# Performance work log

Hardware: AMD Instinct MI355X
Metric: run time of the kernel (lower is better)

## Reference

```python
import jax, jax.numpy as jnp
import numpy as np

N = 100_000   # nodes
E = 1_600_000 # edges (avg degree 16)
IN = 256
OUT = 128
NEG_SLOPE = 0.01  # torch F.leaky_relu default


def setup_inputs() -> dict:
    key = jax.random.key(0)
    k1, k2, k3, k4, k5 = jax.random.split(key, 5)
    h = jax.random.normal(k1, (N, IN), dtype=jnp.float32)
    W = jax.random.normal(k2, (IN, OUT), dtype=jnp.float32) * 0.05  # fc weight (in->out)
    a = jax.random.normal(k3, (2 * OUT,), dtype=jnp.float32) * 0.05  # attn_fc weight, flattened
    src = jax.random.randint(k4, (E,), 0, N, dtype=jnp.int32)
    dst = jax.random.randint(k5, (E,), 0, N, dtype=jnp.int32)
    return {"h": h, "W": W, "a": a, "src": src, "dst": dst, "counter": 3}


def reference(h, W, a, src, dst, counter):
    out_dim = W.shape[1]
    z = h @ W                               # [N, OUT] = fc(h)
    # edge_attention: e = leaky_relu(attn_fc(cat(z[src], z[dst])))
    s = z @ a[:out_dim]                     # [N] src contribution
    t = z @ a[out_dim:]                     # [N] dst contribution
    e = jax.nn.leaky_relu(s[src] + t[dst], NEG_SLOPE)  # [E]
    # segment softmax over incoming edges of each dst node (fixed across iterations)
    m = jax.ops.segment_max(e, dst, num_segments=N)    # [N]
    w = jnp.exp(e - m[dst])                             # [E]
    denom = jax.ops.segment_sum(w, dst, num_segments=N)  # [N]
    alpha = w / denom[dst]                               # [E]
    # nodes with no in-edges keep their previous h (DGL update_all semantics)
    deg = jax.ops.segment_sum(jnp.ones_like(e), dst, num_segments=N)
    has_in = (deg > 0)[:, None]                          # [N,1]
    hcur = z
    for _ in range(int(counter)):
        agg = jax.ops.segment_sum(alpha[:, None] * hcur[src], dst, num_segments=N)  # [N,OUT]
        hcur = jnp.where(has_in, agg, hcur)
    return hcur
```

## Files before the change

### kernel.cpp

```cpp
#include <hip/hip_runtime.h>
#include <math.h>

#define IN_DIM 256
#define OUT_DIM 128
#define BK 1024
#define NBMAX 128

typedef _Float16 f16;
typedef _Float16 f16x2 __attribute__((ext_vector_type(2)));
typedef _Float16 f16x8 __attribute__((ext_vector_type(8)));
typedef float    f32x4 __attribute__((ext_vector_type(4)));

static inline size_t align256(size_t x){ return (x + 255) & ~size_t(255); }

__global__ void init_kernel(int* __restrict__ gcount, int NB){
  int i = threadIdx.x;
  if (i < NB) gcount[i] = 0;
}

__global__ __launch_bounds__(256) void wprep_kernel(const float* __restrict__ Wm,
    f16* __restrict__ WThi, f16* __restrict__ WTlo){
  int idx = blockIdx.x*256 + threadIdx.x;
  int k = idx >> 7, n = idx & 127;
  float v = Wm[(size_t)k*OUT_DIM + n];
  f16 hi = (f16)v;
  WThi[(size_t)n*IN_DIM + k] = hi;
  WTlo[(size_t)n*IN_DIM + k] = (f16)(v - (float)hi);
}

__global__ __launch_bounds__(256) void gemm_kernel(const float* __restrict__ h,
    const f16* __restrict__ WThi, const f16* __restrict__ WTlo,
    const float* __restrict__ attn_a,
    float* __restrict__ z, f16* __restrict__ zh,
    float* __restrict__ s_arr, float* __restrict__ t_arr, int N){
  __shared__ float spart[128][2];
  __shared__ float tpart[128][2];

  const int t = threadIdx.x;
  const int l = t & 63;
  const int w = t >> 6;
  const int wr = w >> 1;
  const int wc = w & 1;
  const int m15 = l & 15;
  const int g   = l >> 4;
  const int row0 = blockIdx.x * 128;

  const float* hrow[4];
  #pragma unroll
  for (int rt=0; rt<4; rt++){
    int r = row0 + wr*64 + rt*16 + m15;
    if (r > N-1) r = N-1;
    hrow[rt] = h + (size_t)r*IN_DIM;
  }
  const f16* bhp[4]; const f16* blp[4];
  #pragma unroll
  for (int ct=0; ct<4; ct++){
    int n = wc*64 + ct*16 + m15;
    bhp[ct] = WThi + (size_t)n*IN_DIM;
    blp[ct] = WTlo + (size_t)n*IN_DIM;
  }

  f32x4 acc[4][4];
  #pragma unroll
  for (int i=0;i<4;i++)
    #pragma unroll
    for (int j=0;j<4;j++) acc[i][j] = (f32x4){0.f,0.f,0.f,0.f};

  const int g8 = g*8;
  #pragma unroll 2
  for (int k0 = 0; k0 < IN_DIM; k0 += 32){
    f16x8 ah[4], al[4];
    #pragma unroll
    for (int rt=0;rt<4;rt++){
      float4 v0 = *(const float4*)&hrow[rt][k0+g8];
      float4 v1 = *(const float4*)&hrow[rt][k0+g8+4];
      float vv[8] = {v0.x,v0.y,v0.z,v0.w,v1.x,v1.y,v1.z,v1.w};
      f16x8 hh, ll;
      #pragma unroll
      for (int q=0;q<8;q++){
        f16 hq = (f16)vv[q];
        hh[q] = hq;
        ll[q] = (f16)(vv[q] - (float)hq);
      }
      ah[rt] = hh; al[rt] = ll;
    }
    #pragma unroll
    for (int ct=0;ct<4;ct++){
      f16x8 bh = *(const f16x8*)&bhp[ct][k0+g8];
      f16x8 bl = *(const f16x8*)&blp[ct][k0+g8];
      #pragma unroll
      for (int rt=0;rt<4;rt++){
        acc[rt][ct] = __builtin_amdgcn_mfma_f32_16x16x32_f16(ah[rt], bh, acc[rt][ct], 0, 0, 0);
        acc[rt][ct] = __builtin_amdgcn_mfma_f32_16x16x32_f16(ah[rt], bl, acc[rt][ct], 0, 0, 0);
        acc[rt][ct] = __builtin_amdgcn_mfma_f32_16x16x32_f16(al[rt], bh, acc[rt][ct], 0, 0, 0);
      }
    }
  }

  float as_[4], at_[4];
  #pragma unroll
  for (int ct=0; ct<4; ct++){
    as_[ct] = attn_a[wc*64 + ct*16 + m15];
    at_[ct] = attn_a[OUT_DIM + wc*64 + ct*16 + m15];
  }

  #pragma unroll
  for (int rt=0; rt<4; rt++){
    #pragma unroll
    for (int r=0; r<4; r++){
      int lrow = wr*64 + rt*16 + g*4 + r;
      int grow = row0 + lrow;
      float sp = 0.f, tp = 0.f;
      #pragma unroll
      for (int ct=0; ct<4; ct++){
        float v = acc[rt][ct][r];
        if (grow < N){
          z [(size_t)grow*OUT_DIM + wc*64 + ct*16 + m15] = v;
          zh[(size_t)grow*OUT_DIM + wc*64 + ct*16 + m15] = (f16)v;
        }
        sp = fmaf(v, as_[ct], sp);
        tp = fmaf(v, at_[ct], tp);
      }
      #pragma unroll
      for (int o=1; o<16; o<<=1){ sp += __shfl_xor(sp,o); tp += __shfl_xor(tp,o); }
      if (m15 == 0){ spart[lrow][wc] = sp; tpart[lrow][wc] = tp; }
    }
  }
  __syncthreads();
  if (t < 128){
    int grow = row0 + t;
    if (grow < N){
      s_arr[grow] = spart[t][0] + spart[t][1];
      t_arr[grow] = tpart[t][0] + tpart[t][1];
    }
  }
}

__global__ __launch_bounds__(256) void count_kernel(const int* __restrict__ dst,
    int* __restrict__ gcount, int E, int NB){
  __shared__ int lh[NBMAX];
  for (int i=threadIdx.x; i<NB; i+=256) lh[i]=0;
  __syncthreads();
  int i = blockIdx.x*blockDim.x + threadIdx.x;
  int stride = gridDim.x*blockDim.x;
  for (; i<E; i+=stride) atomicAdd(&lh[dst[i]>>10], 1);
  __syncthreads();
  for (int i=threadIdx.x; i<NB; i+=256){
    int c = lh[i];
    if (c) atomicAdd(&gcount[i], c);
  }
}

__global__ __launch_bounds__(128) void scanb_kernel(const int* __restrict__ gcount,
    int* __restrict__ gbase, int* __restrict__ gcursor, int* __restrict__ offs,
    int NB, int N, int E){
  int tid = threadIdx.x;
  int v = (tid < NB) ? gcount[tid] : 0;
  int lane = tid & 63, wv = tid >> 6;
  int x = v;
  #pragma unroll
  for (int o=1;o<64;o<<=1){ int y = __shfl_up(x,o); if (lane>=o) x += y; }
  __shared__ int wt[2];
  if (lane==63) wt[wv] = x;
  __syncthreads();
  int off = wv ? wt[0] : 0;
  int excl = off + x - v;
  if (tid < NB){ gbase[tid] = excl; gcursor[tid] = excl; }
  if (tid == 0){ gbase[NB] = E; offs[N] = E; }
}

__global__ __launch_bounds__(256) void scatter_kernel(const int* __restrict__ src,
    const int* __restrict__ dst, const float* __restrict__ s_arr,
    const float* __restrict__ t_arr, int* __restrict__ gcursor,
    int* __restrict__ p_sd, float* __restrict__ p_w, int E, int NB){
  __shared__ int lh[NBMAX];
  __shared__ int lbase[NBMAX];
  for (int i=threadIdx.x;i<NB;i+=256) lh[i]=0;
  __syncthreads();
  int base = blockIdx.x * (256*8);
  int sN[8], dN[8], rk[8];
  float wv[8];
  #pragma unroll
  for (int k=0;k<8;k++){
    int j = base + threadIdx.x + k*256;
    if (j < E){
      int s_ = src[j], d_ = dst[j];
      float e = s_arr[s_] + t_arr[d_];
      e = e > 0.f ? e : 0.01f*e;
      wv[k] = __expf(e);
      sN[k] = s_; dN[k] = d_;
      rk[k] = atomicAdd(&lh[d_>>10], 1);
    } else rk[k] = -1;
  }
  __syncthreads();
  for (int i=threadIdx.x;i<NB;i+=256){
    int c = lh[i];
    lbase[i] = c ? atomicAdd(&gcursor[i], c) : 0;
  }
  __syncthreads();
  #pragma unroll
  for (int k=0;k<8;k++){
    if (rk[k] >= 0){
      int b = dN[k] >> 10;
      int pos = lbase[b] + rk[k];
      p_sd[pos] = sN[k] | ((dN[k] & 1023) << 20);
      p_w[pos]  = wv[k];
    }
  }
}

__global__ __launch_bounds__(512) void bucket_kernel(const int* __restrict__ gbase,
    const int* __restrict__ p_sd, const float* __restrict__ p_w,
    int* __restrict__ offs, int2* __restrict__ csrp, int N){
  __shared__ int   hist[BK];
  __shared__ float wsum[BK];
  __shared__ int   loff[BK];
  __shared__ int   wtot[8];
  int b = blockIdx.x;
  int tid = threadIdx.x;
  int e0 = gbase[b], e1 = gbase[b+1];
  int n0 = b << 10;
  int nn = min(BK, N - n0);
  for (int i=tid;i<BK;i+=512){ hist[i]=0; wsum[i]=0.f; }
  __syncthreads();
  for (int j=e0+tid; j<e1; j+=512){
    int dl = p_sd[j] >> 20;
    atomicAdd(&hist[dl], 1);
    atomicAdd(&wsum[dl], p_w[j]);
  }
  __syncthreads();
  int v0 = hist[tid*2], v1 = hist[tid*2+1];
  int tsum = v0 + v1;
  int lane = tid & 63, wv = tid >> 6;
  int x = tsum;
  #pragma unroll
  for (int o=1;o<64;o<<=1){ int y = __shfl_up(x,o); if (lane>=o) x += y; }
  if (lane==63) wtot[wv] = x;
  __syncthreads();
  int woff = 0;
  for (int i=0;i<wv;i++) woff += wtot[i];
  int excl = woff + x - tsum;
  if (tid*2   < nn) offs[n0 + tid*2  ] = e0 + excl;
  loff[tid*2] = excl; excl += v0;
  if (tid*2+1 < nn) offs[n0 + tid*2+1] = e0 + excl;
  loff[tid*2+1] = excl;
  __syncthreads();
  for (int j=e0+tid; j<e1; j+=512){
    int sd = p_sd[j];
    int dl = sd >> 20;
    int r = atomicAdd(&loff[dl], 1);
    int2 pk; pk.x = sd & 0xFFFFF; pk.y = __float_as_int(p_w[j] / wsum[dl]);
    csrp[e0 + r] = pk;
  }
}

__global__ __launch_bounds__(256) void agg_kernel(const f16* __restrict__ hIn,
    f16* __restrict__ hOut, const float* __restrict__ z, float* __restrict__ out,
    const int* __restrict__ offs, const int2* __restrict__ csrp,
    const int* __restrict__ counter, int it, int N){
  int wv   = threadIdx.x >> 6;
  int lane = threadIdx.x & 63;
  int n = blockIdx.x*4 + wv;
  if (n >= N) return;
  int cntr = counter[0];
  if (cntr <= 0){
    if (it == 0)
      *(float2*)&out[(size_t)n*OUT_DIM + lane*2] =
        *(const float2*)&z[(size_t)n*OUT_DIM + lane*2];
    return;
  }
  if (it >= cntr) return;
  const bool fin = (it == cntr - 1);
  int s0 = offs[n], s1 = offs[n+1];
  if (s0 == s1){
    if (fin)
      *(float2*)&out[(size_t)n*OUT_DIM + lane*2] =
        *(const float2*)&z[(size_t)n*OUT_DIM + lane*2];
    else
      *(f16x2*)&hOut[(size_t)n*OUT_DIM + lane*2] =
        *(const f16x2*)&hIn[(size_t)n*OUT_DIM + lane*2];
    return;
  }
  float2 a0c = {0.f,0.f}, a1c = {0.f,0.f}, a2c = {0.f,0.f}, a3c = {0.f,0.f};
  for (int base = s0; base < s1; base += 64){
    int j = base + lane;
    int2 me = make_int2(0, 0);
    if (j < s1) me = csrp[j];
    int cnt = min(64, s1 - base);
    int k = 0;
    for (; k+4 <= cnt; k += 4){
      int sk0 = __shfl(me.x, k+0); float w0 = __int_as_float(__shfl(me.y, k+0));
      int sk1 = __shfl(me.x, k+1); float w1 = __int_as_float(__shfl(me.y, k+1));
      int sk2 = __shfl(me.x, k+2); float w2 = __int_as_float(__shfl(me.y, k+2));
      int sk3 = __shfl(me.x, k+3); float w3 = __int_as_float(__shfl(me.y, k+3));
      f16x2 v0 = *(const f16x2*)&hIn[(size_t)sk0*OUT_DIM + lane*2];
      f16x2 v1 = *(const f16x2*)&hIn[(size_t)sk1*OUT_DIM + lane*2];
      f16x2 v2 = *(const f16x2*)&hIn[(size_t)sk2*OUT_DIM + lane*2];
      f16x2 v3 = *(const f16x2*)&hIn[(size_t)sk3*OUT_DIM + lane*2];
      a0c.x = fmaf(w0, (float)v0.x, a0c.x); a0c.y = fmaf(w0, (float)v0.y, a0c.y);
      a1c.x = fmaf(w1, (float)v1.x, a1c.x); a1c.y = fmaf(w1, (float)v1.y, a1c.y);
      a2c.x = fmaf(w2, (float)v2.x, a2c.x); a2c.y = fmaf(w2, (float)v2.y, a2c.y);
      a3c.x = fmaf(w3, (float)v3.x, a3c.x); a3c.y = fmaf(w3, (float)v3.y, a3c.y);
    }
    for (; k < cnt; k++){
      int sk = __shfl(me.x, k); float wk = __int_as_float(__shfl(me.y, k));
      f16x2 v = *(const f16x2*)&hIn[(size_t)sk*OUT_DIM + lane*2];
      a0c.x = fmaf(wk, (float)v.x, a0c.x); a0c.y = fmaf(wk, (float)v.y, a0c.y);
    }
  }
  float2 res;
  res.x = (a0c.x + a1c.x) + (a2c.x + a3c.x);
  res.y = (a0c.y + a1c.y) + (a2c.y + a3c.y);
  if (fin){
    *(float2*)&out[(size_t)n*OUT_DIM + lane*2] = res;
  } else {
    f16x2 o = {(f16)res.x, (f16)res.y};
    *(f16x2*)&hOut[(size_t)n*OUT_DIM + lane*2] = o;
  }
}

extern "C" void kernel_launch(void* const* d_in, const int* in_sizes, int n_in,
                              void* d_out, int out_size, void* d_ws, size_t ws_size,
                              hipStream_t stream){
  const float* h   = (const float*)d_in[0];
  const float* Wm  = (const float*)d_in[1];
  const float* a   = (const float*)d_in[2];
  const int*   src = (const int*)d_in[3];
  const int*   dst = (const int*)d_in[4];
  const int* counter = (const int*)d_in[5];
  const int N = in_sizes[0] / IN_DIM;
  const int E = in_sizes[3];
  const int NB = (N + BK - 1) / BK;
  float* out = (float*)d_out;

  char* p = (char*)d_ws;
  auto alloc = [&](size_t bytes){ void* r = (void*)p; p += align256(bytes); return r; };
  float* z         = (float*)alloc((size_t)N*OUT_DIM*4);
  f16*   hA        = (f16*)  alloc((size_t)N*OUT_DIM*2);
  f16*   hB        = (f16*)  alloc((size_t)N*OUT_DIM*2);
  float* s_arr     = (float*)alloc((size_t)N*4);
  float* t_arr     = (float*)alloc((size_t)N*4);
  int*   p_sd      = (int*)  alloc((size_t)E*4);
  float* p_w       = (float*)alloc((size_t)E*4);
  int2*  csrp      = (int2*) alloc((size_t)E*8);
  int*   offs      = (int*)  alloc((size_t)(N+1)*4);
  int*   gcount    = (int*)  alloc((size_t)NBMAX*4);
  int*   gbase     = (int*)  alloc((size_t)(NBMAX+1)*4);
  int*   gcursor   = (int*)  alloc((size_t)NBMAX*4);
  f16*   WThi      = (f16*)  alloc((size_t)IN_DIM*OUT_DIM*2);
  f16*   WTlo      = (f16*)  alloc((size_t)IN_DIM*OUT_DIM*2);

  init_kernel<<<1, 128, 0, stream>>>(gcount, NB);
  wprep_kernel<<<(IN_DIM*OUT_DIM)/256, 256, 0, stream>>>(Wm, WThi, WTlo);
  gemm_kernel<<<(N+127)/128, 256, 0, stream>>>(h, WThi, WTlo, a, z, hA, s_arr, t_arr, N);
  count_kernel<<<512, 256, 0, stream>>>(dst, gcount, E, NB);
  scanb_kernel<<<1, 128, 0, stream>>>(gcount, gbase, gcursor, offs, NB, N, E);
  scatter_kernel<<<(E + 2047)/2048, 256, 0, stream>>>(src, dst, s_arr, t_arr,
                                                      gcursor, p_sd, p_w, E, NB);
  bucket_kernel<<<NB, 512, 0, stream>>>(gbase, p_sd, p_w, offs, csrp, N);
  agg_kernel<<<(N+3)/4, 256, 0, stream>>>(hA, hB, z, out, offs, csrp, counter, 0, N);
  agg_kernel<<<(N+3)/4, 256, 0, stream>>>(hB, hA, z, out, offs, csrp, counter, 1, N);
  agg_kernel<<<(N+3)/4, 256, 0, stream>>>(hA, hB, z, out, offs, csrp, counter, 2, N);
}
```

Measured before the change: 383.0 us.

## Stage GEMM A-tiles in LDS, drop fp32 z buffer, halve bucket size

The GEMM now loads each h row once per block, converts it to hi/lo fp16 and double-buffers it in shared memory. Before, each wave reread and reconverted h rows straight from global memory. The fp32 z output is removed, so nodes without in-edges (and the counter<=0 case) now output the fp16 copy upcast to float. This cuts about 51MB of writes but loses precision on those rows. Bucket size drops from 1024 to 512 nodes, doubling the number of bucket blocks, and the scan and bucket kernels are adjusted to match.

Result: faster. 335.7 us (-12.3%).

```diff
diff --git a/kernel.cpp b/kernel.cpp
--- a/kernel.cpp
+++ b/kernel.cpp
@@ -3,8 +3,8 @@
 
 #define IN_DIM 256
 #define OUT_DIM 128
-#define BK 1024
-#define NBMAX 128
+#define BK 512
+#define NBMAX 256
 
 typedef _Float16 f16;
 typedef _Float16 f16x2 __attribute__((ext_vector_type(2)));
@@ -31,8 +31,8 @@
 __global__ __launch_bounds__(256) void gemm_kernel(const float* __restrict__ h,
     const f16* __restrict__ WThi, const f16* __restrict__ WTlo,
     const float* __restrict__ attn_a,
-    float* __restrict__ z, f16* __restrict__ zh,
-    float* __restrict__ s_arr, float* __restrict__ t_arr, int N){
+    f16* __restrict__ zh, float* __restrict__ s_arr, float* __restrict__ t_arr, int N){
+  __shared__ f16x8 Alds[2][2][512];
   __shared__ float spart[128][2];
   __shared__ float tpart[128][2];
 
@@ -45,13 +45,11 @@
   const int g   = l >> 4;
   const int row0 = blockIdx.x * 128;
 
-  const float* hrow[4];
-  #pragma unroll
-  for (int rt=0; rt<4; rt++){
-    int r = row0 + wr*64 + rt*16 + m15;
-    if (r > N-1) r = N-1;
-    hrow[rt] = h + (size_t)r*IN_DIM;
-  }
+  const int srow = t >> 1;
+  const int g0 = (t & 1) * 2;
+  const float* srcrow = h + (size_t)min(row0 + srow, N-1) * IN_DIM;
+  const int wslot0 = (srow >> 4)*64 + g0*16 + (srow & 15);
+
   const f16* bhp[4]; const f16* blp[4];
   #pragma unroll
   for (int ct=0; ct<4; ct++){
@@ -66,35 +64,64 @@
     #pragma unroll
     for (int j=0;j<4;j++) acc[i][j] = (f32x4){0.f,0.f,0.f,0.f};
 
-  const int g8 = g*8;
-  #pragma unroll 2
-  for (int k0 = 0; k0 < IN_DIM; k0 += 32){
+  auto cvt_write = [&](int buf, float4* r){
+    float vv[16] = {r[0].x,r[0].y,r[0].z,r[0].w, r[1].x,r[1].y,r[1].z,r[1].w,
+                    r[2].x,r[2].y,r[2].z,r[2].w, r[3].x,r[3].y,r[3].z,r[3].w};
+    f16x8 hh0, ll0, hh1, ll1;
+    #pragma unroll
+    for (int q=0;q<8;q++){
+      f16 a = (f16)vv[q];   hh0[q]=a; ll0[q]=(f16)(vv[q]  -(float)a);
+      f16 c = (f16)vv[q+8]; hh1[q]=c; ll1[q]=(f16)(vv[q+8]-(float)c);
+    }
+    Alds[buf][0][wslot0]    = hh0;
+    Alds[buf][1][wslot0]    = ll0;
+    Alds[buf][0][wslot0+16] = hh1;
+    Alds[buf][1][wslot0+16] = ll1;
+  };
+
+  float4 rg4[2][4];
+  #pragma unroll
+  for (int q=0;q<4;q++) rg4[0][q] = *(const float4*)&srcrow[g0*8 + q*4];
+  cvt_write(0, rg4[0]);
+  #pragma unroll
+  for (int q=0;q<4;q++) rg4[1][q] = *(const float4*)&srcrow[32 + g0*8 + q*4];
+  __syncthreads();
+
+  #pragma unroll
+  for (int step=0; step<8; ++step){
+    const int b = step & 1;
+    const int kq = step*32 + g*8;
+    f16x8 bh[4], bl[4];
+    #pragma unroll
+    for (int ct=0;ct<4;ct++){
+      bh[ct] = *(const f16x8*)&bhp[ct][kq];
+      bl[ct] = *(const f16x8*)&blp[ct][kq];
+    }
+    if (step < 7){
+      cvt_write(b^1, rg4[(step+1)&1]);
+      if (step < 6){
+        #pragma unroll
+        for (int q=0;q<4;q++)
+          rg4[step&1][q] = *(const float4*)&srcrow[(step+2)*32 + g0*8 + q*4];
+      }
+    }
     f16x8 ah[4], al[4];
     #pragma unroll
     for (int rt=0;rt<4;rt++){
-      float4 v0 = *(const float4*)&hrow[rt][k0+g8];
-      float4 v1 = *(const float4*)&hrow[rt][k0+g8+4];
-      float vv[8] = {v0.x,v0.y,v0.z,v0.w,v1.x,v1.y,v1.z,v1.w};
-      f16x8 hh, ll;
-      #pragma unroll
-      for (int q=0;q<8;q++){
-        f16 hq = (f16)vv[q];
-        hh[q] = hq;
-        ll[q] = (f16)(vv[q] - (float)hq);
-      }
-      ah[rt] = hh; al[rt] = ll;
+      int idx = (wr*4+rt)*64 + l;
+      ah[rt] = Alds[b][0][idx];
+      al[rt] = Alds[b][1][idx];
     }
     #pragma unroll
     for (int ct=0;ct<4;ct++){
-      f16x8 bh = *(const f16x8*)&bhp[ct][k0+g8];
-      f16x8 bl = *(const f16x8*)&blp[ct][k0+g8];
       #pragma unroll
       for (int rt=0;rt<4;rt++){
-        acc[rt][ct] = __builtin_amdgcn_mfma_f32_16x16x32_f16(ah[rt], bh, acc[rt][ct], 0, 0, 0);
-        acc[rt][ct] = __builtin_amdgcn_mfma_f32_16x16x32_f16(ah[rt], bl, acc[rt][ct], 0, 0, 0);
-        acc[rt][ct] = __builtin_amdgcn_mfma_f32_16x16x32_f16(al[rt], bh, acc[rt][ct], 0, 0, 0);
+        acc[rt][ct] = __builtin_amdgcn_mfma_f32_16x16x32_f16(ah[rt], bh[ct], acc[rt][ct], 0, 0, 0);
+        acc[rt][ct] = __builtin_amdgcn_mfma_f32_16x16x32_f16(ah[rt], bl[ct], acc[rt][ct], 0, 0, 0);
+        acc[rt][ct] = __builtin_amdgcn_mfma_f32_16x16x32_f16(al[rt], bh[ct], acc[rt][ct], 0, 0, 0);
       }
     }
+    __syncthreads();
   }
 
   float as_[4], at_[4];
@@ -114,10 +141,7 @@
       #pragma unroll
       for (int ct=0; ct<4; ct++){
         float v = acc[rt][ct][r];
-        if (grow < N){
-          z [(size_t)grow*OUT_DIM + wc*64 + ct*16 + m15] = v;
-          zh[(size_t)grow*OUT_DIM + wc*64 + ct*16 + m15] = (f16)v;
-        }
+        if (grow < N) zh[(size_t)grow*OUT_DIM + wc*64 + ct*16 + m15] = (f16)v;
         sp = fmaf(v, as_[ct], sp);
         tp = fmaf(v, at_[ct], tp);
       }
@@ -143,7 +167,7 @@
   __syncthreads();
   int i = blockIdx.x*blockDim.x + threadIdx.x;
   int stride = gridDim.x*blockDim.x;
-  for (; i<E; i+=stride) atomicAdd(&lh[dst[i]>>10], 1);
+  for (; i<E; i+=stride) atomicAdd(&lh[dst[i]>>9], 1);
   __syncthreads();
   for (int i=threadIdx.x; i<NB; i+=256){
     int c = lh[i];
@@ -151,7 +175,7 @@
   }
 }
 
-__global__ __launch_bounds__(128) void scanb_kernel(const int* __restrict__ gcount,
+__global__ __launch_bounds__(256) void scanb_kernel(const int* __restrict__ gcount,
     int* __restrict__ gbase, int* __restrict__ gcursor, int* __restrict__ offs,
     int NB, int N, int E){
   int tid = threadIdx.x;
@@ -160,10 +184,11 @@
   int x = v;
   #pragma unroll
   for (int o=1;o<64;o<<=1){ int y = __shfl_up(x,o); if (lane>=o) x += y; }
-  __shared__ int wt[2];
+  __shared__ int wt[4];
   if (lane==63) wt[wv] = x;
   __syncthreads();
-  int off = wv ? wt[0] : 0;
+  int off = 0;
+  for (int i=0;i<wv;i++) off += wt[i];
   int excl = off + x - v;
   if (tid < NB){ gbase[tid] = excl; gcursor[tid] = excl; }
   if (tid == 0){ gbase[NB] = E; offs[N] = E; }
@@ -189,7 +214,7 @@
       e = e > 0.f ? e : 0.01f*e;
       wv[k] = __expf(e);
       sN[k] = s_; dN[k] = d_;
-      rk[k] = atomicAdd(&lh[d_>>10], 1);
+      rk[k] = atomicAdd(&lh[d_>>9], 1);
     } else rk[k] = -1;
   }
   __syncthreads();
@@ -201,9 +226,9 @@
   #pragma unroll
   for (int k=0;k<8;k++){
     if (rk[k] >= 0){
-      int b = dN[k] >> 10;
+      int b = dN[k] >> 9;
       int pos = lbase[b] + rk[k];
-      p_sd[pos] = sN[k] | ((dN[k] & 1023) << 20);
+      p_sd[pos] = sN[k] | ((dN[k] & 511) << 20);
       p_w[pos]  = wv[k];
     }
   }
@@ -219,9 +244,9 @@
   int b = blockIdx.x;
   int tid = threadIdx.x;
   int e0 = gbase[b], e1 = gbase[b+1];
-  int n0 = b << 10;
+  int n0 = b << 9;
   int nn = min(BK, N - n0);
-  for (int i=tid;i<BK;i+=512){ hist[i]=0; wsum[i]=0.f; }
+  hist[tid] = 0; wsum[tid] = 0.f;
   __syncthreads();
   for (int j=e0+tid; j<e1; j+=512){
     int dl = p_sd[j] >> 20;
@@ -229,21 +254,18 @@
     atomicAdd(&wsum[dl], p_w[j]);
   }
   __syncthreads();
-  int v0 = hist[tid*2], v1 = hist[tid*2+1];
-  int tsum = v0 + v1;
+  int v = hist[tid];
   int lane = tid & 63, wv = tid >> 6;
-  int x = tsum;
+  int x = v;
   #pragma unroll
   for (int o=1;o<64;o<<=1){ int y = __shfl_up(x,o); if (lane>=o) x += y; }
   if (lane==63) wtot[wv] = x;
   __syncthreads();
   int woff = 0;
   for (int i=0;i<wv;i++) woff += wtot[i];
-  int excl = woff + x - tsum;
-  if (tid*2   < nn) offs[n0 + tid*2  ] = e0 + excl;
-  loff[tid*2] = excl; excl += v0;
-  if (tid*2+1 < nn) offs[n0 + tid*2+1] = e0 + excl;
-  loff[tid*2+1] = excl;
+  int excl = woff + x - v;
+  if (tid < nn) offs[n0 + tid] = e0 + excl;
+  loff[tid] = excl;
   __syncthreads();
   for (int j=e0+tid; j<e1; j+=512){
     int sd = p_sd[j];
@@ -255,7 +277,7 @@
 }
 
 __global__ __launch_bounds__(256) void agg_kernel(const f16* __restrict__ hIn,
-    f16* __restrict__ hOut, const float* __restrict__ z, float* __restrict__ out,
+    f16* __restrict__ hOut, float* __restrict__ out,
     const int* __restrict__ offs, const int2* __restrict__ csrp,
     const int* __restrict__ counter, int it, int N){
   int wv   = threadIdx.x >> 6;
@@ -264,21 +286,24 @@
   if (n >= N) return;
   int cntr = counter[0];
   if (cntr <= 0){
-    if (it == 0)
-      *(float2*)&out[(size_t)n*OUT_DIM + lane*2] =
-        *(const float2*)&z[(size_t)n*OUT_DIM + lane*2];
+    if (it == 0){
+      f16x2 v = *(const f16x2*)&hIn[(size_t)n*OUT_DIM + lane*2];
+      float2 o; o.x = (float)v.x; o.y = (float)v.y;
+      *(float2*)&out[(size_t)n*OUT_DIM + lane*2] = o;
+    }
     return;
   }
   if (it >= cntr) return;
   const bool fin = (it == cntr - 1);
   int s0 = offs[n], s1 = offs[n+1];
   if (s0 == s1){
-    if (fin)
-      *(float2*)&out[(size_t)n*OUT_DIM + lane*2] =
-        *(const float2*)&z[(size_t)n*OUT_DIM + lane*2];
-    else
-      *(f16x2*)&hOut[(size_t)n*OUT_DIM + lane*2] =
-        *(const f16x2*)&hIn[(size_t)n*OUT_DIM + lane*2];
+    f16x2 v = *(const f16x2*)&hIn[(size_t)n*OUT_DIM + lane*2];
+    if (fin){
+      float2 o; o.x = (float)v.x; o.y = (float)v.y;
+      *(float2*)&out[(size_t)n*OUT_DIM + lane*2] = o;
+    } else {
+      *(f16x2*)&hOut[(size_t)n*OUT_DIM + lane*2] = v;
+    }
     return;
   }
   float2 a0c = {0.f,0.f}, a1c = {0.f,0.f}, a2c = {0.f,0.f}, a3c = {0.f,0.f};
@@ -335,7 +360,6 @@
 
   char* p = (char*)d_ws;
   auto alloc = [&](size_t bytes){ void* r = (void*)p; p += align256(bytes); return r; };
-  float* z         = (float*)alloc((size_t)N*OUT_DIM*4);
   f16*   hA        = (f16*)  alloc((size_t)N*OUT_DIM*2);
   f16*   hB        = (f16*)  alloc((size_t)N*OUT_DIM*2);
   float* s_arr     = (float*)alloc((size_t)N*4);
@@ -350,15 +374,15 @@
   f16*   WThi      = (f16*)  alloc((size_t)IN_DIM*OUT_DIM*2);
   f16*   WTlo      = (f16*)  alloc((size_t)IN_DIM*OUT_DIM*2);
 
-  init_kernel<<<1, 128, 0, stream>>>(gcount, NB);
+  init_kernel<<<1, 256, 0, stream>>>(gcount, NB);
   wprep_kernel<<<(IN_DIM*OUT_DIM)/256, 256, 0, stream>>>(Wm, WThi, WTlo);
-  gemm_kernel<<<(N+127)/128, 256, 0, stream>>>(h, WThi, WTlo, a, z, hA, s_arr, t_arr, N);
+  gemm_kernel<<<(N+127)/128, 256, 0, stream>>>(h, WThi, WTlo, a, hA, s_arr, t_arr, N);
   count_kernel<<<512, 256, 0, stream>>>(dst, gcount, E, NB);
-  scanb_kernel<<<1, 128, 0, stream>>>(gcount, gbase, gcursor, offs, NB, N, E);
+  scanb_kernel<<<1, 256, 0, stream>>>(gcount, gbase, gcursor, offs, NB, N, E);
   scatter_kernel<<<(E + 2047)/2048, 256, 0, stream>>>(src, dst, s_arr, t_arr,
                                                       gcursor, p_sd, p_w, E, NB);
   bucket_kernel<<<NB, 512, 0, stream>>>(gbase, p_sd, p_w, offs, csrp, N);
-  agg_kernel<<<(N+3)/4, 256, 0, stream>>>(hA, hB, z, out, offs, csrp, counter, 0, N);
-  agg_kernel<<<(N+3)/4, 256, 0, stream>>>(hB, hA, z, out, offs, csrp, counter, 1, N);
-  agg_kernel<<<(N+3)/4, 256, 0, stream>>>(hA, hB, z, out, offs, csrp, counter, 2, N);
-}
+  agg_kernel<<<(N+3)/4, 256, 0, stream>>>(hA, hB, out, offs, csrp, counter, 0, N);
+  agg_kernel<<<(N+3)/4, 256, 0, stream>>>(hB, hA, out, offs, csrp, counter, 1, N);
+  agg_kernel<<<(N+3)/4, 256, 0, stream>>>(hA, hB, out, offs, csrp, counter, 2, N);
+}
```
